# Kernel optimization log

Hardware: AMD Instinct MI355X
Metric: run time of the kernel (lower is better)

The kernel has to match this reference:

```python
import jax, jax.numpy as jnp
import numpy as np

EPS = 1e-6  # config.normalization_layer_epsilon

def setup_inputs() -> dict:
    key = jax.random.key(0)
    k1, k2 = jax.random.split(key)
    B, S, G, D, K = 4, 4096, 4, 1024, 4
    x = jax.random.normal(k1, (B, S, G, D), dtype=jnp.float32)
    norm_scale = jnp.ones((G, D), dtype=jnp.float32)  # per-branch RMSNorm scales (stacked by nnx.vmap)
    conv_kernel = jax.random.normal(k2, (K, G * D), dtype=jnp.float32) * 0.1  # depthwise taps per channel
    return {"x": x, "norm_scale": norm_scale, "conv_kernel": conv_kernel}

def reference(x, norm_scale, conv_kernel):
    B, S, G, D = x.shape
    K, C = conv_kernel.shape  # C == G * D
    # Per-branch RMSNorm over last dim D (scale broadcasts over [G, D])
    ms = jnp.mean(jnp.square(x), axis=-1, keepdims=True)
    xn = x * jax.lax.rsqrt(ms + EPS) * norm_scale  # (B, S, G, D)
    xf = xn.reshape(B, S, C)
    # Causal depthwise conv1d: left-pad (K-1), feature_group_count = C
    xp = jnp.pad(xf, ((0, 0), (K - 1, 0), (0, 0)))
    y = jax.lax.conv_general_dilated(
        xp,
        conv_kernel[:, None, :],  # (W, I=1, O=C)
        window_strides=(1,),
        padding='VALID',
        dimension_numbers=('NWC', 'WIO', 'NWC'),
        feature_group_count=C,
    )  # (B, S, C)
    y = jax.nn.silu(y)
    return y.reshape(B, S, G, D)
```

## Files before the change

kernel.cpp:

```cpp
#include <hip/hip_runtime.h>
#include <math.h>

constexpr int B = 4;
constexpr int S = 4096;
constexpr int G = 4;
constexpr int D = 1024;
constexpr int K = 4;
constexpr int C = G * D;
constexpr int CHUNK = 64;
constexpr float EPS = 1e-6f;

__global__ __launch_bounds__(256)
void shortconv_fused_kernel(const float* __restrict__ x,
                            const float* __restrict__ scale,
                            const float* __restrict__ w,
                            float* __restrict__ out)
{
    __shared__ float red[2][4];

    const int tid  = threadIdx.x;
    const int lane = tid & 63;
    const int wid  = tid >> 6;
    const int bg   = blockIdx.y;
    const int b    = bg >> 2;
    const int g    = bg & 3;
    const int s0   = blockIdx.x * CHUNK;
    const int d0   = tid * 4;

    const size_t srow = (size_t)G * D;
    const size_t base = (size_t)b * S * srow + (size_t)g * D + d0;

    const float4 sc = *(const float4*)(scale + g * D + d0);
    const float4 w0 = *(const float4*)(w + 0 * C + g * D + d0);
    const float4 w1 = *(const float4*)(w + 1 * C + g * D + d0);
    const float4 w2 = *(const float4*)(w + 2 * C + g * D + d0);
    const float4 w3 = *(const float4*)(w + 3 * C + g * D + d0);

    float4 win0 = make_float4(0.f, 0.f, 0.f, 0.f);
    float4 win1 = make_float4(0.f, 0.f, 0.f, 0.f);
    float4 win2 = make_float4(0.f, 0.f, 0.f, 0.f);

    int s = s0 - (K - 1);
    float4 xv_next;
    if (s >= 0) xv_next = *(const float4*)(x + base + (size_t)s * srow);
    else        xv_next = make_float4(0.f, 0.f, 0.f, 0.f);

    const int s_end = s0 + CHUNK;
    for (; s < s_end; ++s) {
        float4 xv = xv_next;
        const int sn = s + 1;
        if (sn < s_end) {
            xv_next = (sn >= 0) ? *(const float4*)(x + base + (size_t)sn * srow)
                                : make_float4(0.f, 0.f, 0.f, 0.f);
        }

        float local = xv.x * xv.x + xv.y * xv.y + xv.z * xv.z + xv.w * xv.w;
        #pragma unroll
        for (int off = 32; off > 0; off >>= 1)
            local += __shfl_xor(local, off, 64);
        const int buf = s & 1;
        if (lane == 0) red[buf][wid] = local;
        __syncthreads();
        const float total = red[buf][0] + red[buf][1] + red[buf][2] + red[buf][3];
        const float invr  = rsqrtf(total * (1.0f / D) + EPS);

        float4 nv;
        nv.x = xv.x * invr * sc.x;
        nv.y = xv.y * invr * sc.y;
        nv.z = xv.z * invr * sc.z;
        nv.w = xv.w * invr * sc.w;

        if (s >= s0) {
            float4 y;
            y.x = w0.x * win0.x + w1.x * win1.x + w2.x * win2.x + w3.x * nv.x;
            y.y = w0.y * win0.y + w1.y * win1.y + w2.y * win2.y + w3.y * nv.y;
            y.z = w0.z * win0.z + w1.z * win1.z + w2.z * win2.z + w3.z * nv.z;
            y.w = w0.w * win0.w + w1.w * win1.w + w2.w * win2.w + w3.w * nv.w;
            y.x = y.x / (1.f + __expf(-y.x));
            y.y = y.y / (1.f + __expf(-y.y));
            y.z = y.z / (1.f + __expf(-y.z));
            y.w = y.w / (1.f + __expf(-y.w));
            *(float4*)(out + base + (size_t)s * srow) = y;
        }

        win0 = win1;
        win1 = win2;
        win2 = nv;
    }
}

extern "C" void kernel_launch(void* const* d_in, const int* in_sizes, int n_in,
                              void* d_out, int out_size, void* d_ws, size_t ws_size,
                              hipStream_t stream) {
    const float* x     = (const float*)d_in[0];
    const float* scale = (const float*)d_in[1];
    const float* w     = (const float*)d_in[2];
    float* out         = (float*)d_out;

    dim3 grid(S / CHUNK, B * G);
    dim3 block(256);
    shortconv_fused_kernel<<<grid, block, 0, stream>>>(x, scale, w, out);
}
```

Measured before the change: 110.2 us.

## Process two timesteps per iteration to halve block barriers, with nontemporal stores

New measurement: 106.6 us. 3.2% less time.

```diff
diff --git a/kernel.cpp b/kernel.cpp
--- a/kernel.cpp
+++ b/kernel.cpp
@@ -10,13 +10,15 @@
 constexpr int CHUNK = 64;
 constexpr float EPS = 1e-6f;
 
+typedef float v4f __attribute__((ext_vector_type(4)));
+
 __global__ __launch_bounds__(256)
 void shortconv_fused_kernel(const float* __restrict__ x,
                             const float* __restrict__ scale,
                             const float* __restrict__ w,
                             float* __restrict__ out)
 {
-    __shared__ float red[2][4];
+    __shared__ float red[2][2][4];
 
     const int tid  = threadIdx.x;
     const int lane = tid & 63;
@@ -36,56 +38,75 @@
     const float4 w2 = *(const float4*)(w + 2 * C + g * D + d0);
     const float4 w3 = *(const float4*)(w + 3 * C + g * D + d0);
 
-    float4 win0 = make_float4(0.f, 0.f, 0.f, 0.f);
-    float4 win1 = make_float4(0.f, 0.f, 0.f, 0.f);
-    float4 win2 = make_float4(0.f, 0.f, 0.f, 0.f);
+    const float4 zero = make_float4(0.f, 0.f, 0.f, 0.f);
 
-    int s = s0 - (K - 1);
-    float4 xv_next;
-    if (s >= 0) xv_next = *(const float4*)(x + base + (size_t)s * srow);
-    else        xv_next = make_float4(0.f, 0.f, 0.f, 0.f);
+    float4 win0 = zero, win1 = zero, win2 = zero;
+
+    int s = s0 - 4;
+    float4 cur0 = (s     >= 0) ? *(const float4*)(x + base + (size_t)(s    ) * srow) : zero;
+    float4 cur1 = (s + 1 >= 0) ? *(const float4*)(x + base + (size_t)(s + 1) * srow) : zero;
 
     const int s_end = s0 + CHUNK;
-    for (; s < s_end; ++s) {
-        float4 xv = xv_next;
-        const int sn = s + 1;
-        if (sn < s_end) {
-            xv_next = (sn >= 0) ? *(const float4*)(x + base + (size_t)sn * srow)
-                                : make_float4(0.f, 0.f, 0.f, 0.f);
+    for (; s < s_end; s += 2) {
+        float4 nxt0 = zero, nxt1 = zero;
+        if (s + 2 < s_end) {
+            if (s + 2 >= 0) nxt0 = *(const float4*)(x + base + (size_t)(s + 2) * srow);
+            if (s + 3 >= 0) nxt1 = *(const float4*)(x + base + (size_t)(s + 3) * srow);
         }
 
-        float local = xv.x * xv.x + xv.y * xv.y + xv.z * xv.z + xv.w * xv.w;
+        float l0 = cur0.x * cur0.x + cur0.y * cur0.y + cur0.z * cur0.z + cur0.w * cur0.w;
+        float l1 = cur1.x * cur1.x + cur1.y * cur1.y + cur1.z * cur1.z + cur1.w * cur1.w;
         #pragma unroll
-        for (int off = 32; off > 0; off >>= 1)
-            local += __shfl_xor(local, off, 64);
-        const int buf = s & 1;
-        if (lane == 0) red[buf][wid] = local;
+        for (int off = 32; off > 0; off >>= 1) {
+            l0 += __shfl_xor(l0, off, 64);
+            l1 += __shfl_xor(l1, off, 64);
+        }
+        const int buf = (s >> 1) & 1;
+        if (lane == 0) {
+            red[buf][0][wid] = l0;
+            red[buf][1][wid] = l1;
+        }
         __syncthreads();
-        const float total = red[buf][0] + red[buf][1] + red[buf][2] + red[buf][3];
-        const float invr  = rsqrtf(total * (1.0f / D) + EPS);
+        const float t0 = red[buf][0][0] + red[buf][0][1] + red[buf][0][2] + red[buf][0][3];
+        const float t1 = red[buf][1][0] + red[buf][1][1] + red[buf][1][2] + red[buf][1][3];
+        const float invr0 = rsqrtf(t0 * (1.0f / D) + EPS);
+        const float invr1 = rsqrtf(t1 * (1.0f / D) + EPS);
 
-        float4 nv;
-        nv.x = xv.x * invr * sc.x;
-        nv.y = xv.y * invr * sc.y;
-        nv.z = xv.z * invr * sc.z;
-        nv.w = xv.w * invr * sc.w;
+        float4 nv0, nv1;
+        nv0.x = cur0.x * invr0 * sc.x;  nv0.y = cur0.y * invr0 * sc.y;
+        nv0.z = cur0.z * invr0 * sc.z;  nv0.w = cur0.w * invr0 * sc.w;
+        nv1.x = cur1.x * invr1 * sc.x;  nv1.y = cur1.y * invr1 * sc.y;
+        nv1.z = cur1.z * invr1 * sc.z;  nv1.w = cur1.w * invr1 * sc.w;
 
         if (s >= s0) {
-            float4 y;
-            y.x = w0.x * win0.x + w1.x * win1.x + w2.x * win2.x + w3.x * nv.x;
-            y.y = w0.y * win0.y + w1.y * win1.y + w2.y * win2.y + w3.y * nv.y;
-            y.z = w0.z * win0.z + w1.z * win1.z + w2.z * win2.z + w3.z * nv.z;
-            y.w = w0.w * win0.w + w1.w * win1.w + w2.w * win2.w + w3.w * nv.w;
-            y.x = y.x / (1.f + __expf(-y.x));
-            y.y = y.y / (1.f + __expf(-y.y));
-            y.z = y.z / (1.f + __expf(-y.z));
-            y.w = y.w / (1.f + __expf(-y.w));
-            *(float4*)(out + base + (size_t)s * srow) = y;
+            float4 y0, y1;
+            y0.x = w0.x * win0.x + w1.x * win1.x + w2.x * win2.x + w3.x * nv0.x;
+            y0.y = w0.y * win0.y + w1.y * win1.y + w2.y * win2.y + w3.y * nv0.y;
+            y0.z = w0.z * win0.z + w1.z * win1.z + w2.z * win2.z + w3.z * nv0.z;
+            y0.w = w0.w * win0.w + w1.w * win1.w + w2.w * win2.w + w3.w * nv0.w;
+            y1.x = w0.x * win1.x + w1.x * win2.x + w2.x * nv0.x + w3.x * nv1.x;
+            y1.y = w0.y * win1.y + w1.y * win2.y + w2.y * nv0.y + w3.y * nv1.y;
+            y1.z = w0.z * win1.z + w1.z * win2.z + w2.z * nv0.z + w3.z * nv1.z;
+            y1.w = w0.w * win1.w + w1.w * win2.w + w2.w * nv0.w + w3.w * nv1.w;
+            y0.x *= __builtin_amdgcn_rcpf(1.f + __expf(-y0.x));
+            y0.y *= __builtin_amdgcn_rcpf(1.f + __expf(-y0.y));
+            y0.z *= __builtin_amdgcn_rcpf(1.f + __expf(-y0.z));
+            y0.w *= __builtin_amdgcn_rcpf(1.f + __expf(-y0.w));
+            y1.x *= __builtin_amdgcn_rcpf(1.f + __expf(-y1.x));
+            y1.y *= __builtin_amdgcn_rcpf(1.f + __expf(-y1.y));
+            y1.z *= __builtin_amdgcn_rcpf(1.f + __expf(-y1.z));
+            y1.w *= __builtin_amdgcn_rcpf(1.f + __expf(-y1.w));
+            v4f yv0 = { y0.x, y0.y, y0.z, y0.w };
+            v4f yv1 = { y1.x, y1.y, y1.z, y1.w };
+            __builtin_nontemporal_store(yv0, (v4f*)(out + base + (size_t)(s    ) * srow));
+            __builtin_nontemporal_store(yv1, (v4f*)(out + base + (size_t)(s + 1) * srow));
         }
 
-        win0 = win1;
-        win1 = win2;
-        win2 = nv;
+        win0 = win2;
+        win1 = nv0;
+        win2 = nv1;
+        cur0 = nxt0;
+        cur1 = nxt1;
     }
 }
 
```

## Give each wavefront a full row strip to drop block-level reductions

Applied to the files above, without the earlier changes.

New measurement: 88.83 us. 1.24x faster.

```diff
diff --git a/kernel.cpp b/kernel.cpp
--- a/kernel.cpp
+++ b/kernel.cpp
@@ -7,85 +7,101 @@
 constexpr int D = 1024;
 constexpr int K = 4;
 constexpr int C = G * D;
-constexpr int CHUNK = 64;
+constexpr int STRIP = 32;
 constexpr float EPS = 1e-6f;
 
+typedef float v4f __attribute__((ext_vector_type(4)));
+
 __global__ __launch_bounds__(256)
-void shortconv_fused_kernel(const float* __restrict__ x,
-                            const float* __restrict__ scale,
-                            const float* __restrict__ w,
-                            float* __restrict__ out)
+void shortconv_wave_kernel(const float* __restrict__ x,
+                           const float* __restrict__ scale,
+                           const float* __restrict__ w,
+                           float* __restrict__ out)
 {
-    __shared__ float red[2][4];
+    const int tid   = threadIdx.x;
+    const int lane  = tid & 63;
+    const int wid   = tid >> 6;
+    const int gw    = blockIdx.x * 4 + wid;
+    const int nstr  = S / STRIP;
+    const int strip = gw & (nstr - 1);
+    const int bg    = gw >> 7;
+    const int b     = bg >> 2;
+    const int g     = bg & 3;
+    const int s0    = strip * STRIP;
+    const int send  = s0 + STRIP;
 
-    const int tid  = threadIdx.x;
-    const int lane = tid & 63;
-    const int wid  = tid >> 6;
-    const int bg   = blockIdx.y;
-    const int b    = bg >> 2;
-    const int g    = bg & 3;
-    const int s0   = blockIdx.x * CHUNK;
-    const int d0   = tid * 4;
+    const size_t base = (size_t)b * S * C + (size_t)g * D + (size_t)(lane * 4);
+    const int    coff = g * D + lane * 4;
 
-    const size_t srow = (size_t)G * D;
-    const size_t base = (size_t)b * S * srow + (size_t)g * D + d0;
+    v4f sc[4], wt0[4], wt1[4], wt2[4], wt3[4];
+    #pragma unroll
+    for (int j = 0; j < 4; ++j) {
+        sc[j]  = *(const v4f*)(scale + coff + j * 256);
+        wt0[j] = *(const v4f*)(w + 0 * C + coff + j * 256);
+        wt1[j] = *(const v4f*)(w + 1 * C + coff + j * 256);
+        wt2[j] = *(const v4f*)(w + 2 * C + coff + j * 256);
+        wt3[j] = *(const v4f*)(w + 3 * C + coff + j * 256);
+    }
 
-    const float4 sc = *(const float4*)(scale + g * D + d0);
-    const float4 w0 = *(const float4*)(w + 0 * C + g * D + d0);
-    const float4 w1 = *(const float4*)(w + 1 * C + g * D + d0);
-    const float4 w2 = *(const float4*)(w + 2 * C + g * D + d0);
-    const float4 w3 = *(const float4*)(w + 3 * C + g * D + d0);
+    v4f win0[4], win1[4], win2[4], cur[4], nxt[4];
+    #pragma unroll
+    for (int j = 0; j < 4; ++j) {
+        win0[j] = (v4f)0.f; win1[j] = (v4f)0.f; win2[j] = (v4f)0.f;
+        nxt[j] = (v4f)0.f;
+    }
 
-    float4 win0 = make_float4(0.f, 0.f, 0.f, 0.f);
-    float4 win1 = make_float4(0.f, 0.f, 0.f, 0.f);
-    float4 win2 = make_float4(0.f, 0.f, 0.f, 0.f);
+    {
+        const int s = s0 - 3;
+        #pragma unroll
+        for (int j = 0; j < 4; ++j)
+            cur[j] = (s >= 0) ? *(const v4f*)(x + base + (size_t)s * C + j * 256)
+                              : (v4f)0.f;
+    }
 
-    int s = s0 - (K - 1);
-    float4 xv_next;
-    if (s >= 0) xv_next = *(const float4*)(x + base + (size_t)s * srow);
-    else        xv_next = make_float4(0.f, 0.f, 0.f, 0.f);
-
-    const int s_end = s0 + CHUNK;
-    for (; s < s_end; ++s) {
-        float4 xv = xv_next;
+    for (int s = s0 - 3; s < send; ++s) {
         const int sn = s + 1;
-        if (sn < s_end) {
-            xv_next = (sn >= 0) ? *(const float4*)(x + base + (size_t)sn * srow)
-                                : make_float4(0.f, 0.f, 0.f, 0.f);
+        if (sn < send) {
+            #pragma unroll
+            for (int j = 0; j < 4; ++j)
+                nxt[j] = (sn >= 0) ? *(const v4f*)(x + base + (size_t)sn * C + j * 256)
+                                   : (v4f)0.f;
         }
 
-        float local = xv.x * xv.x + xv.y * xv.y + xv.z * xv.z + xv.w * xv.w;
+        v4f a = cur[0] * cur[0];
+        a += cur[1] * cur[1];
+        a += cur[2] * cur[2];
+        a += cur[3] * cur[3];
+        float local = a.x + a.y + a.z + a.w;
         #pragma unroll
         for (int off = 32; off > 0; off >>= 1)
             local += __shfl_xor(local, off, 64);
-        const int buf = s & 1;
-        if (lane == 0) red[buf][wid] = local;
-        __syncthreads();
-        const float total = red[buf][0] + red[buf][1] + red[buf][2] + red[buf][3];
-        const float invr  = rsqrtf(total * (1.0f / D) + EPS);
+        const float invr = rsqrtf(local * (1.0f / D) + EPS);
 
-        float4 nv;
-        nv.x = xv.x * invr * sc.x;
-        nv.y = xv.y * invr * sc.y;
-        nv.z = xv.z * invr * sc.z;
-        nv.w = xv.w * invr * sc.w;
+        v4f nv[4];
+        #pragma unroll
+        for (int j = 0; j < 4; ++j)
+            nv[j] = cur[j] * (invr * sc[j]);
 
         if (s >= s0) {
-            float4 y;
-            y.x = w0.x * win0.x + w1.x * win1.x + w2.x * win2.x + w3.x * nv.x;
-            y.y = w0.y * win0.y + w1.y * win1.y + w2.y * win2.y + w3.y * nv.y;
-            y.z = w0.z * win0.z + w1.z * win1.z + w2.z * win2.z + w3.z * nv.z;
-            y.w = w0.w * win0.w + w1.w * win1.w + w2.w * win2.w + w3.w * nv.w;
-            y.x = y.x / (1.f + __expf(-y.x));
-            y.y = y.y / (1.f + __expf(-y.y));
-            y.z = y.z / (1.f + __expf(-y.z));
-            y.w = y.w / (1.f + __expf(-y.w));
-            *(float4*)(out + base + (size_t)s * srow) = y;
+            #pragma unroll
+            for (int j = 0; j < 4; ++j) {
+                v4f y = wt0[j] * win0[j] + wt1[j] * win1[j]
+                      + wt2[j] * win2[j] + wt3[j] * nv[j];
+                y.x *= __builtin_amdgcn_rcpf(1.f + __expf(-y.x));
+                y.y *= __builtin_amdgcn_rcpf(1.f + __expf(-y.y));
+                y.z *= __builtin_amdgcn_rcpf(1.f + __expf(-y.z));
+                y.w *= __builtin_amdgcn_rcpf(1.f + __expf(-y.w));
+                __builtin_nontemporal_store(y, (v4f*)(out + base + (size_t)s * C + j * 256));
+            }
         }
 
-        win0 = win1;
-        win1 = win2;
-        win2 = nv;
+        #pragma unroll
+        for (int j = 0; j < 4; ++j) {
+            win0[j] = win1[j];
+            win1[j] = win2[j];
+            win2[j] = nv[j];
+            cur[j]  = nxt[j];
+        }
     }
 }
 
@@ -97,7 +113,8 @@
     const float* w     = (const float*)d_in[2];
     float* out         = (float*)d_out;
 
-    dim3 grid(S / CHUNK, B * G);
+    const int total_waves = (S / STRIP) * B * G;
+    dim3 grid(total_waves / 4);
     dim3 block(256);
-    shortconv_fused_kernel<<<grid, block, 0, stream>>>(x, scale, w, out);
+    shortconv_wave_kernel<<<grid, block, 0, stream>>>(x, scale, w, out);
 }
```
